# Performance work log

Hardware: AMD Instinct MI355X
Metric: run time of the kernel (lower is better)

The kernel has to match this reference:

```python
import jax, jax.numpy as jnp
import numpy as np

B, P, H, A = 256, 196, 1024, 512

def setup_inputs() -> dict:
    key = jax.random.key(0)
    ks = jax.random.split(key, 20)
    s = 1.0 / np.sqrt(H)
    sa = 1.0 / np.sqrt(A)
    return {
        "spatial_image": jax.random.normal(ks[0], (B, P, H), jnp.float32),
        "decoder_out": jax.random.normal(ks[1], (B, H), jnp.float32),
        "st": jax.random.normal(ks[2], (B, H), jnp.float32),
        "W_sen_aff": jax.random.uniform(ks[3], (H, H), jnp.float32, -s, s),
        "b_sen_aff": jax.random.uniform(ks[4], (H,), jnp.float32, -s, s),
        "W_sen_att": jax.random.uniform(ks[5], (H, A), jnp.float32, -s, s),
        "b_sen_att": jax.random.uniform(ks[6], (A,), jnp.float32, -s, s),
        "W_h_aff": jax.random.uniform(ks[7], (H, H), jnp.float32, -s, s),
        "b_h_aff": jax.random.uniform(ks[8], (H,), jnp.float32, -s, s),
        "W_h_att": jax.random.uniform(ks[9], (H, A), jnp.float32, -s, s),
        "b_h_att": jax.random.uniform(ks[10], (A,), jnp.float32, -s, s),
        "W_v_att": jax.random.uniform(ks[11], (H, A), jnp.float32, -s, s),
        "b_v_att": jax.random.uniform(ks[12], (A,), jnp.float32, -s, s),
        "W_alpha": jax.random.uniform(ks[13], (A, 1), jnp.float32, -sa, sa),
        "b_alpha": jax.random.uniform(ks[14], (1,), jnp.float32, -sa, sa),
        "W_ctx": jax.random.uniform(ks[15], (H, H), jnp.float32, -s, s),
        "b_ctx": jax.random.uniform(ks[16], (H,), jnp.float32, -s, s),
    }

def reference(spatial_image, decoder_out, st,
              W_sen_aff, b_sen_aff, W_sen_att, b_sen_att,
              W_h_aff, b_h_aff, W_h_att, b_h_att,
              W_v_att, b_v_att, W_alpha, b_alpha, W_ctx, b_ctx):
    # visual_attn: [B, P, A]
    visual_attn = jnp.einsum('bph,ha->bpa', spatial_image, W_v_att) + b_v_att
    # sentinel path: [B, H] -> relu affine -> [B, A]
    sentinel_affine = jax.nn.relu(st @ W_sen_aff + b_sen_aff)
    sentinel_attn = sentinel_affine @ W_sen_att + b_sen_att
    # hidden path: [B, H] -> tanh affine -> [B, A]
    hidden_affine = jnp.tanh(decoder_out @ W_h_aff + b_h_aff)
    hidden_attn = hidden_affine @ W_h_att + b_h_att
    # concat sentinel as an extra "pixel": [B, P+1, H] and [B, P+1, A]
    concat_features = jnp.concatenate([spatial_image, sentinel_affine[:, None, :]], axis=1)
    attended_features = jnp.concatenate([visual_attn, sentinel_attn[:, None, :]], axis=1)
    attention = jnp.tanh(attended_features + hidden_attn[:, None, :])  # [B, P+1, A]
    alpha = (jnp.einsum('bpa,ao->bpo', attention, W_alpha) + b_alpha)[..., 0]  # [B, P+1]
    att_weights = jax.nn.softmax(alpha, axis=1)
    context = jnp.einsum('bph,bp->bh', concat_features, att_weights)  # [B, H]
    beta_value = att_weights[:, -1:]  # [B, 1]
    out_l = jnp.tanh((context + hidden_affine) @ W_ctx + b_ctx)  # [B, H]
    return (out_l, att_weights, beta_value)
```

## Files before the change

kernel.cpp:

```cpp
#include <hip/hip_runtime.h>
#include <hip/hip_bf16.h>
#include <stdint.h>
#include <stddef.h>

typedef __attribute__((ext_vector_type(4))) float f32x4;
typedef __attribute__((ext_vector_type(8))) short short8;

#define MROWS 50176


static __device__ __forceinline__ int lds_off(int row, int k) {
    int slot = (k >> 3) ^ ((row >> 1) & 3);
    return (row << 6) + (slot << 4) + ((k & 7) << 1);
}

static __device__ __forceinline__ unsigned div196(unsigned g) {
    return (unsigned)(((unsigned long long)g * 85599ull) >> 24);
}

static __device__ __forceinline__ unsigned short f2bf(float f) {
    union { float f; unsigned u; } v; v.f = f;
    unsigned r = v.u + 0x7FFFu + ((v.u >> 16) & 1u);
    return (unsigned short)(r >> 16);
}

static __device__ __forceinline__ unsigned long long pack4bf(f32x4 a) {
    union { unsigned long long u; __hip_bfloat162 h[2]; } r;
    r.h[0] = __float22bfloat162_rn(make_float2(a[0], a[1]));
    r.h[1] = __float22bfloat162_rn(make_float2(a[2], a[3]));
    return r.u;
}

static __device__ __forceinline__ float tanh_fast(float x) {
    float xc = fminf(fmaxf(x, -9.f), 9.f);
    float e = __builtin_amdgcn_exp2f(xc * 2.885390081777927f);
    return (e - 1.f) * __builtin_amdgcn_rcpf(e + 1.f);
}

static __device__ __forceinline__ void gload_lds16(const void* g, void* l) {
    __builtin_amdgcn_global_load_lds(
        (const __attribute__((address_space(1))) unsigned int*)g,
        (__attribute__((address_space(3))) unsigned int*)l, 16, 0, 0);
}

__global__ __launch_bounds__(512, 2) void attn_alpha_kernel(
    const float* __restrict__ spatial,
    const unsigned short* __restrict__ WvT,
    const float* __restrict__ b_v_att,
    const float* __restrict__ hidden_attn,
    const float* __restrict__ W_alpha,
    float* __restrict__ alphab)
{
    __shared__ char sA[2][8192];
    __shared__ char sB[2][32768];
    float* alpha_s = (float*)&sA[0][0];
    const int tid = threadIdx.x;
    const int row0 = blockIdx.x << 7;

    const int lane = tid & 63, w = tid >> 6;
    const int wr = w >> 2, wc = w & 3;
    const int lrow = lane & 15, lk = lane >> 4;

    const int arow = tid >> 3;
    const int acol = (tid & 7) << 2;
    const float* Ap = spatial + (size_t)(row0 + arow) * 1024 + acol;
    const int aoff0 = lds_off(arow, acol);
    const int aoff1 = lds_off(arow + 64, acol);

    const int kg = (lane & 3) ^ ((lane >> 3) & 3);
    const unsigned short* Bp = WvT + (size_t)((w << 4) + (lane >> 2)) * 1024 + (kg << 3);

    f32x4 acc[4][8];
    f32x4 z = {0.f, 0.f, 0.f, 0.f};
    #pragma unroll
    for (int m = 0; m < 4; ++m)
        #pragma unroll
        for (int n = 0; n < 8; ++n) acc[m][n] = z;

    {
        f32x4 a0 = *(const f32x4*)(Ap);
        f32x4 a1 = *(const f32x4*)(Ap + 64 * 1024);
        #pragma unroll
        for (int r = 0; r < 4; ++r)
            gload_lds16(Bp + ((size_t)r << 17), sB[0] + (r << 13) + (w << 10));
        *(unsigned long long*)(sA[0] + aoff0) = pack4bf(a0);
        *(unsigned long long*)(sA[0] + aoff1) = pack4bf(a1);
    }
    __syncthreads();

    int cur = 0;
    #pragma unroll 1
    for (int ks = 0; ks < 32; ++ks) {
        const int nxt = cur ^ 1;
        f32x4 a0n, a1n;
        if (ks < 31) {
            const float* Apk = Ap + ((ks + 1) << 5);
            a0n = *(const f32x4*)(Apk);
            a1n = *(const f32x4*)(Apk + 64 * 1024);
            const unsigned short* Bpk = Bp + ((ks + 1) << 5);
            #pragma unroll
            for (int r = 0; r < 4; ++r)
                gload_lds16(Bpk + ((size_t)r << 17), sB[nxt] + (r << 13) + (w << 10));
        }
        short8 af[4], bf[8];
        #pragma unroll
        for (int m = 0; m < 4; ++m)
            af[m] = *(const short8*)(sA[cur] + lds_off((wr << 6) + (m << 4) + lrow, lk << 3));
        #pragma unroll
        for (int n = 0; n < 8; ++n)
            bf[n] = *(const short8*)(sB[cur] + lds_off((wc << 7) + (n << 4) + lrow, lk << 3));
        __builtin_amdgcn_s_setprio(1);
        #pragma unroll
        for (int m = 0; m < 4; ++m)
            #pragma unroll
            for (int n = 0; n < 8; ++n)
                acc[m][n] = __builtin_amdgcn_mfma_f32_16x16x32_bf16(af[m], bf[n], acc[m][n], 0, 0, 0);
        __builtin_amdgcn_s_setprio(0);
        if (ks < 31) {
            *(unsigned long long*)(sA[nxt] + aoff0) = pack4bf(a0n);
            *(unsigned long long*)(sA[nxt] + aoff1) = pack4bf(a1n);
        }
        __syncthreads();
        cur = nxt;
    }

    if (tid < 128) alpha_s[tid] = 0.f;
    __syncthreads();

    const unsigned bb0 = div196((unsigned)row0);
    const unsigned bb1 = div196((unsigned)(row0 + 127));
    float bv[8], wa[8], h0[8], h1[8];
    #pragma unroll
    for (int n = 0; n < 8; ++n) {
        int g = (wc << 7) + (n << 4) + lrow;
        bv[n] = b_v_att[g];
        wa[n] = W_alpha[g];
        h0[n] = hidden_attn[bb0 * 512 + g];
        h1[n] = hidden_attn[bb1 * 512 + g];
    }
    #pragma unroll
    for (int m = 0; m < 4; ++m) {
        int rloc0 = (wr << 6) + (m << 4) + (lk << 2);
        #pragma unroll
        for (int i = 0; i < 4; ++i) {
            unsigned g = (unsigned)(row0 + rloc0 + i);
            bool first = (div196(g) == bb0);
            float s = 0.f;
            #pragma unroll
            for (int n = 0; n < 8; ++n) {
                float v = tanh_fast(acc[m][n][i] + bv[n] + (first ? h0[n] : h1[n]));
                s += v * wa[n];
            }
            #pragma unroll
            for (int off = 1; off < 16; off <<= 1) s += __shfl_xor(s, off);
            if (lrow == 0) atomicAdd(&alpha_s[rloc0 + i], s);
        }
    }
    __syncthreads();
    if (tid < 128) {
        unsigned g = (unsigned)(row0 + tid);
        unsigned bb = div196(g);
        unsigned p = g - bb * 196;
        alphab[bb * 196 + p] = alpha_s[tid];
    }
}

static __device__ __forceinline__ void kloop_dbuf(
    const float* __restrict__ Abase,
    const unsigned short* __restrict__ Bbase,
    char* sA0, char* sA1, char* sB0, char* sB1,
    f32x4 acc[4][4], int tid)
{
    const int lane = tid & 63, w = tid >> 6;
    const int lrow = lane & 15, lk = lane >> 4;
    const int wr = w >> 1, wc = w & 1;

    const float* Ap[4];
    int aoff[4];
    #pragma unroll
    for (int r = 0; r < 4; ++r) {
        int q = tid + (r << 8);
        int ar = q >> 3, kc = (q & 7) << 2;
        Ap[r] = Abase + (size_t)ar * 1024 + kc;
        aoff[r] = lds_off(ar, kc);
    }
    const unsigned short* Bp[2];
    int bdst[2];
    #pragma unroll
    for (int c = 0; c < 2; ++c) {
        int ch = (w << 1) + c;
        int row = (ch << 4) + (lane >> 2);
        int kg = (lane & 3) ^ ((row >> 1) & 3);
        Bp[c] = Bbase + (size_t)row * 1024 + (kg << 3);
        bdst[c] = ch << 10;
    }

    f32x4 z = {0.f, 0.f, 0.f, 0.f};
    #pragma unroll
    for (int m = 0; m < 4; ++m)
        #pragma unroll
        for (int n = 0; n < 4; ++n) acc[m][n] = z;

    {
        f32x4 a[4];
        #pragma unroll
        for (int r = 0; r < 4; ++r) a[r] = *(const f32x4*)Ap[r];
        #pragma unroll
        for (int c = 0; c < 2; ++c) gload_lds16(Bp[c], sB0 + bdst[c]);
        #pragma unroll
        for (int r = 0; r < 4; ++r)
            *(unsigned long long*)(sA0 + aoff[r]) = pack4bf(a[r]);
    }
    __syncthreads();

    char* sAc = sA0; char* sAn = sA1;
    char* sBc = sB0; char* sBn = sB1;
    for (int ks = 0; ks < 32; ++ks) {
        f32x4 an[4];
        if (ks < 31) {
            const int ko = (ks + 1) << 5;
            #pragma unroll
            for (int r = 0; r < 4; ++r) an[r] = *(const f32x4*)(Ap[r] + ko);
            #pragma unroll
            for (int c = 0; c < 2; ++c) gload_lds16(Bp[c] + ko, sBn + bdst[c]);
        }
        short8 af[4], bf[4];
        #pragma unroll
        for (int m = 0; m < 4; ++m)
            af[m] = *(const short8*)(sAc + lds_off((wr << 6) + (m << 4) + lrow, lk << 3));
        #pragma unroll
        for (int n = 0; n < 4; ++n)
            bf[n] = *(const short8*)(sBc + lds_off((wc << 6) + (n << 4) + lrow, lk << 3));
        #pragma unroll
        for (int m = 0; m < 4; ++m)
            #pragma unroll
            for (int n = 0; n < 4; ++n)
                acc[m][n] = __builtin_amdgcn_mfma_f32_16x16x32_bf16(af[m], bf[n], acc[m][n], 0, 0, 0);
        if (ks < 31) {
            #pragma unroll
            for (int r = 0; r < 4; ++r)
                *(unsigned long long*)(sAn + aoff[r]) = pack4bf(an[r]);
        }
        __syncthreads();
        char* t;
        t = sAc; sAc = sAn; sAn = t;
        t = sBc; sBc = sBn; sBn = t;
    }
}

struct GemmDesc { const float* A; const unsigned short* BT; const float* bias; float* C; int N; int act; };
struct GemmPair { GemmDesc d[2]; };

__global__ __launch_bounds__(256, 4) void gemm_pair_kernel(GemmPair p)
{
    GemmDesc d = p.d[blockIdx.z];
    __shared__ char sA[2][8192];
    __shared__ char sB[2][8192];
    const int tid = threadIdx.x;
    const int row0 = blockIdx.x << 7;
    const int col0 = blockIdx.y << 7;
    f32x4 acc[4][4];
    kloop_dbuf(d.A + (size_t)row0 * 1024, d.BT + (size_t)col0 * 1024,
               sA[0], sA[1], sB[0], sB[1], acc, tid);
    const int lane = tid & 63, w = tid >> 6;
    const int wr = w >> 1, wc = w & 1;
    const int lrow = lane & 15, lk = lane >> 4;
    #pragma unroll
    for (int n = 0; n < 4; ++n) {
        int col = col0 + (wc << 6) + (n << 4) + lrow;
        float bs = d.bias[col];
        #pragma unroll
        for (int m = 0; m < 4; ++m) {
            int rbase = row0 + (wr << 6) + (m << 4) + (lk << 2);
            #pragma unroll
            for (int i = 0; i < 4; ++i) {
                float v = acc[m][n][i] + bs;
                if (d.act == 1) v = fmaxf(v, 0.f);
                if (d.act == 2) v = tanh_fast(v);
                d.C[(size_t)(rbase + i) * d.N + col] = v;
            }
        }
    }
}

struct TransDesc { const float* src; unsigned short* dst; int K; int N; };
struct TransArgs { TransDesc d[6]; };

__global__ void transpose_cvt_kernel(TransArgs args) {
    TransDesc d = args.d[blockIdx.y];
    int nt = d.N >> 5;
    int tiles = (d.K >> 5) * nt;
    if ((int)blockIdx.x >= tiles) return;
    int tk = blockIdx.x / nt, tn = blockIdx.x % nt;
    __shared__ unsigned short tile[32][33];
    int tx = threadIdx.x & 31, ty = threadIdx.x >> 5;
    int k0 = tk << 5, n0 = tn << 5;
    #pragma unroll
    for (int j = 0; j < 4; ++j)
        tile[ty + j * 8][tx] = f2bf(d.src[(size_t)(k0 + ty + j * 8) * d.N + n0 + tx]);
    __syncthreads();
    #pragma unroll
    for (int j = 0; j < 4; ++j)
        d.dst[(size_t)(n0 + ty + j * 8) * d.K + k0 + tx] = tile[tx][ty + j * 8];
}

__global__ void softmax_sentinel_kernel(
    const float* __restrict__ alphab,
    const float* __restrict__ sen_att, const float* __restrict__ hid_att,
    const float* __restrict__ W_alpha,
    float* __restrict__ att, float* __restrict__ beta)
{
    int b = blockIdx.x, tid = threadIdx.x;
    __shared__ float al[197];
    __shared__ float red[4];
    if (tid < 196) al[tid] = alphab[b * 196 + tid];
    float s = 0.f;
    for (int a = tid; a < 512; a += 256)
        s += tanh_fast(sen_att[b * 512 + a] + hid_att[b * 512 + a]) * W_alpha[a];
    #pragma unroll
    for (int off = 1; off < 64; off <<= 1) s += __shfl_xor(s, off);
    if ((tid & 63) == 0) red[tid >> 6] = s;
    __syncthreads();
    if (tid == 0) al[196] = red[0] + red[1] + red[2] + red[3];
    __syncthreads();
    if (tid < 64) {
        float v[4];
        float mx = -1e30f;
        #pragma unroll
        for (int jj = 0; jj < 4; ++jj) {
            int i = tid + jj * 64;
            v[jj] = (i < 197) ? al[i] : -1e30f;
            mx = fmaxf(mx, v[jj]);
        }
        #pragma unroll
        for (int off = 1; off < 64; off <<= 1) mx = fmaxf(mx, __shfl_xor(mx, off));
        float sm = 0.f;
        #pragma unroll
        for (int jj = 0; jj < 4; ++jj) {
            v[jj] = __builtin_amdgcn_exp2f((v[jj] - mx) * 1.442695040888963f);
            if (tid + jj * 64 >= 197) v[jj] = 0.f;
            sm += v[jj];
        }
        #pragma unroll
        for (int off = 1; off < 64; off <<= 1) sm += __shfl_xor(sm, off);
        float inv = 1.f / sm;
        #pragma unroll
        for (int jj = 0; jj < 4; ++jj) {
            int i = tid + jj * 64;
            if (i < 197) {
                float wv = v[jj] * inv;
                att[b * 197 + i] = wv;
                if (i == 196) beta[b] = wv;
            }
        }
    }
}

__global__ __launch_bounds__(256) void context_kernel(
    const float* __restrict__ spatial, const float* __restrict__ sen_aff,
    const float* __restrict__ hid_aff, const float* __restrict__ att,
    float* __restrict__ ctxh)
{
    int b = blockIdx.x, half = blockIdx.y, t = threadIdx.x;
    __shared__ float wsm[197];
    if (t < 197) wsm[t] = att[b * 197 + t];
    __syncthreads();
    int h2 = (half << 8) + t;
    const float2* sp = (const float2*)(spatial + (size_t)b * 196 * 1024) + h2;
    float ax = 0.f, ay = 0.f;
    #pragma unroll 8
    for (int p = 0; p < 196; ++p) {
        float2 x = sp[(size_t)p * 512];
        ax += wsm[p] * x.x; ay += wsm[p] * x.y;
    }
    float w196 = wsm[196];
    float2 sa = ((const float2*)(sen_aff + (size_t)b * 1024))[h2];
    float2 ha = ((const float2*)(hid_aff + (size_t)b * 1024))[h2];
    ctxh[(size_t)b * 1024 + 2 * h2]     = ax + w196 * sa.x + ha.x;
    ctxh[(size_t)b * 1024 + 2 * h2 + 1] = ay + w196 * sa.y + ha.y;
}

extern "C" void kernel_launch(void* const* d_in, const int* in_sizes, int n_in,
                              void* d_out, int out_size, void* d_ws, size_t ws_size,
                              hipStream_t stream)
{
    const float* spatial   = (const float*)d_in[0];
    const float* decoder   = (const float*)d_in[1];
    const float* st        = (const float*)d_in[2];
    const float* W_sen_aff = (const float*)d_in[3];
    const float* b_sen_aff = (const float*)d_in[4];
    const float* W_sen_att = (const float*)d_in[5];
    const float* b_sen_att = (const float*)d_in[6];
    const float* W_h_aff   = (const float*)d_in[7];
    const float* b_h_aff   = (const float*)d_in[8];
    const float* W_h_att   = (const float*)d_in[9];
    const float* b_h_att   = (const float*)d_in[10];
    const float* W_v_att   = (const float*)d_in[11];
    const float* b_v_att   = (const float*)d_in[12];
    const float* W_alpha   = (const float*)d_in[13];
    const float* W_ctx     = (const float*)d_in[15];
    const float* b_ctx     = (const float*)d_in[16];

    char* ws = (char*)d_ws;
    size_t off = 0;
    auto alloc = [&](size_t bytes) {
        char* p = ws + off; off += (bytes + 255) & ~(size_t)255; return p;
    };
    unsigned short* WvT  = (unsigned short*)alloc((size_t)512 * 1024 * 2);
    unsigned short* WsaT = (unsigned short*)alloc((size_t)1024 * 1024 * 2);
    unsigned short* WstT = (unsigned short*)alloc((size_t)512 * 1024 * 2);
    unsigned short* WhaT = (unsigned short*)alloc((size_t)1024 * 1024 * 2);
    unsigned short* WhtT = (unsigned short*)alloc((size_t)512 * 1024 * 2);
    unsigned short* WcxT = (unsigned short*)alloc((size_t)1024 * 1024 * 2);
    float* sen_aff = (float*)alloc((size_t)256 * 1024 * 4);
    float* sen_att = (float*)alloc((size_t)256 * 512 * 4);
    float* hid_aff = (float*)alloc((size_t)256 * 1024 * 4);
    float* hid_att = (float*)alloc((size_t)256 * 512 * 4);
    float* alphab  = (float*)alloc((size_t)MROWS * 4);
    float* ctxh    = (float*)alloc((size_t)256 * 1024 * 4);

    float* out_l    = (float*)d_out;
    float* out_att  = out_l + 256 * 1024;
    float* out_beta = out_att + 256 * 197;

    TransArgs ta;
    ta.d[0] = { W_v_att,   WvT,  1024, 512  };
    ta.d[1] = { W_sen_aff, WsaT, 1024, 1024 };
    ta.d[2] = { W_sen_att, WstT, 1024, 512  };
    ta.d[3] = { W_h_aff,   WhaT, 1024, 1024 };
    ta.d[4] = { W_h_att,   WhtT, 1024, 512  };
    ta.d[5] = { W_ctx,     WcxT, 1024, 1024 };
    transpose_cvt_kernel<<<dim3(1024, 6), 256, 0, stream>>>(ta);

    GemmPair p1;
    p1.d[0] = { st,      WsaT, b_sen_aff, sen_aff, 1024, 1 };
    p1.d[1] = { decoder, WhaT, b_h_aff,   hid_aff, 1024, 2 };
    gemm_pair_kernel<<<dim3(2, 8, 2), 256, 0, stream>>>(p1);

    GemmPair p2;
    p2.d[0] = { sen_aff, WstT, b_sen_att, sen_att, 512, 0 };
    p2.d[1] = { hid_aff, WhtT, b_h_att,   hid_att, 512, 0 };
    gemm_pair_kernel<<<dim3(2, 4, 2), 256, 0, stream>>>(p2);

    attn_alpha_kernel<<<392, 512, 0, stream>>>(spatial, WvT, b_v_att, hid_att, W_alpha, alphab);
    softmax_sentinel_kernel<<<256, 256, 0, stream>>>(alphab, sen_att, hid_att, W_alpha, out_att, out_beta);
    context_kernel<<<dim3(256, 2), 256, 0, stream>>>(spatial, sen_aff, hid_aff, out_att, ctxh);

    GemmPair p3;
    p3.d[0] = { ctxh, WcxT, b_ctx, out_l, 1024, 2 };
    p3.d[1] = { ctxh, WcxT, b_ctx, out_l, 1024, 2 };
    gemm_pair_kernel<<<dim3(2, 8, 1), 256, 0, stream>>>(p3);
}
```

Baseline: 240.5 us.

## Shrink attn_alpha tile to 32 rows with register-staged B and more blocks

The visual-attention GEMM block tile drops from 128 to 32 rows, so the grid grows from 392 to 1568 blocks and occupancy is raised to 4 blocks per CU. B (the weight tile) is now staged through registers into a single LDS buffer instead of double-buffered async global-to-LDS loads, and the priority hints are removed, adding an extra barrier per k-step. The aim is to fill more CUs and overlap better, but each block now re-reads the full weight slice per 32 rows, which quadruples weight traffic and lowers MFMA reuse per LDS load.

```diff
diff --git a/kernel.cpp b/kernel.cpp
--- a/kernel.cpp
+++ b/kernel.cpp
@@ -22,6 +22,12 @@
     union { float f; unsigned u; } v; v.f = f;
     unsigned r = v.u + 0x7FFFu + ((v.u >> 16) & 1u);
     return (unsigned short)(r >> 16);
+}
+
+static __device__ __forceinline__ unsigned pack2bf(float2 a) {
+    union { unsigned u; __hip_bfloat162 h; } r;
+    r.h = __float22bfloat162_rn(a);
+    return r.u;
 }
 
 static __device__ __forceinline__ unsigned long long pack4bf(f32x4 a) {
@@ -43,7 +49,7 @@
         (__attribute__((address_space(3))) unsigned int*)l, 16, 0, 0);
 }
 
-__global__ __launch_bounds__(512, 2) void attn_alpha_kernel(
+__global__ __launch_bounds__(512, 4) void attn_alpha_kernel(
     const float* __restrict__ spatial,
     const unsigned short* __restrict__ WvT,
     const float* __restrict__ b_v_att,
@@ -51,113 +57,112 @@
     const float* __restrict__ W_alpha,
     float* __restrict__ alphab)
 {
-    __shared__ char sA[2][8192];
-    __shared__ char sB[2][32768];
+    __shared__ char sA[2][2048];
+    __shared__ char sB[32768];
     float* alpha_s = (float*)&sA[0][0];
     const int tid = threadIdx.x;
-    const int row0 = blockIdx.x << 7;
+    const int row0 = blockIdx.x << 5;
 
     const int lane = tid & 63, w = tid >> 6;
-    const int wr = w >> 2, wc = w & 3;
     const int lrow = lane & 15, lk = lane >> 4;
 
-    const int arow = tid >> 3;
-    const int acol = (tid & 7) << 2;
+    const int arow = tid >> 4;
+    const int acol = (tid & 15) << 1;
     const float* Ap = spatial + (size_t)(row0 + arow) * 1024 + acol;
-    const int aoff0 = lds_off(arow, acol);
-    const int aoff1 = lds_off(arow + 64, acol);
-
-    const int kg = (lane & 3) ^ ((lane >> 3) & 3);
-    const unsigned short* Bp = WvT + (size_t)((w << 4) + (lane >> 2)) * 1024 + (kg << 3);
-
-    f32x4 acc[4][8];
+    const int aoff = lds_off(arow, acol);
+
+    const unsigned short* Bq[4];
+    int boff[4];
+    #pragma unroll
+    for (int c = 0; c < 4; ++c) {
+        int row = (c << 7) + (w << 4) + (lane >> 2);
+        int ke = (lane & 3) << 3;
+        Bq[c] = WvT + (size_t)row * 1024 + ke;
+        boff[c] = lds_off(row, ke);
+    }
+
+    f32x4 acc[2][4];
     f32x4 z = {0.f, 0.f, 0.f, 0.f};
     #pragma unroll
-    for (int m = 0; m < 4; ++m)
-        #pragma unroll
-        for (int n = 0; n < 8; ++n) acc[m][n] = z;
+    for (int m = 0; m < 2; ++m)
+        #pragma unroll
+        for (int n = 0; n < 4; ++n) acc[m][n] = z;
 
     {
-        f32x4 a0 = *(const f32x4*)(Ap);
-        f32x4 a1 = *(const f32x4*)(Ap + 64 * 1024);
-        #pragma unroll
-        for (int r = 0; r < 4; ++r)
-            gload_lds16(Bp + ((size_t)r << 17), sB[0] + (r << 13) + (w << 10));
-        *(unsigned long long*)(sA[0] + aoff0) = pack4bf(a0);
-        *(unsigned long long*)(sA[0] + aoff1) = pack4bf(a1);
-    }
-    __syncthreads();
-
-    int cur = 0;
-    #pragma unroll 1
+        float2 a0 = *(const float2*)Ap;
+        f32x4 b0[4];
+        #pragma unroll
+        for (int c = 0; c < 4; ++c) b0[c] = *(const f32x4*)Bq[c];
+        *(unsigned*)(sA[0] + aoff) = pack2bf(a0);
+        #pragma unroll
+        for (int c = 0; c < 4; ++c) *(f32x4*)(sB + boff[c]) = b0[c];
+    }
+    __syncthreads();
+
     for (int ks = 0; ks < 32; ++ks) {
-        const int nxt = cur ^ 1;
-        f32x4 a0n, a1n;
+        const int cur = ks & 1, nxt = cur ^ 1;
+        float2 aN;
+        f32x4 bN[4];
         if (ks < 31) {
-            const float* Apk = Ap + ((ks + 1) << 5);
-            a0n = *(const f32x4*)(Apk);
-            a1n = *(const f32x4*)(Apk + 64 * 1024);
-            const unsigned short* Bpk = Bp + ((ks + 1) << 5);
-            #pragma unroll
-            for (int r = 0; r < 4; ++r)
-                gload_lds16(Bpk + ((size_t)r << 17), sB[nxt] + (r << 13) + (w << 10));
-        }
-        short8 af[4], bf[8];
-        #pragma unroll
-        for (int m = 0; m < 4; ++m)
-            af[m] = *(const short8*)(sA[cur] + lds_off((wr << 6) + (m << 4) + lrow, lk << 3));
-        #pragma unroll
-        for (int n = 0; n < 8; ++n)
-            bf[n] = *(const short8*)(sB[cur] + lds_off((wc << 7) + (n << 4) + lrow, lk << 3));
-        __builtin_amdgcn_s_setprio(1);
-        #pragma unroll
-        for (int m = 0; m < 4; ++m)
-            #pragma unroll
-            for (int n = 0; n < 8; ++n)
+            const int ko = (ks + 1) << 5;
+            aN = *(const float2*)(Ap + ko);
+            #pragma unroll
+            for (int c = 0; c < 4; ++c) bN[c] = *(const f32x4*)(Bq[c] + ko);
+        }
+        short8 af[2], bf[4];
+        #pragma unroll
+        for (int m = 0; m < 2; ++m)
+            af[m] = *(const short8*)(sA[cur] + lds_off((m << 4) + lrow, lk << 3));
+        #pragma unroll
+        for (int n = 0; n < 4; ++n)
+            bf[n] = *(const short8*)(sB + lds_off((w << 6) + (n << 4) + lrow, lk << 3));
+        #pragma unroll
+        for (int m = 0; m < 2; ++m)
+            #pragma unroll
+            for (int n = 0; n < 4; ++n)
                 acc[m][n] = __builtin_amdgcn_mfma_f32_16x16x32_bf16(af[m], bf[n], acc[m][n], 0, 0, 0);
-        __builtin_amdgcn_s_setprio(0);
+        __syncthreads();
         if (ks < 31) {
-            *(unsigned long long*)(sA[nxt] + aoff0) = pack4bf(a0n);
-            *(unsigned long long*)(sA[nxt] + aoff1) = pack4bf(a1n);
-        }
-        __syncthreads();
-        cur = nxt;
-    }
-
-    if (tid < 128) alpha_s[tid] = 0.f;
+            *(unsigned*)(sA[nxt] + aoff) = pack2bf(aN);
+            #pragma unroll
+            for (int c = 0; c < 4; ++c) *(f32x4*)(sB + boff[c]) = bN[c];
+            __syncthreads();
+        }
+    }
+
+    if (tid < 32) alpha_s[tid] = 0.f;
     __syncthreads();
 
     const unsigned bb0 = div196((unsigned)row0);
-    const unsigned bb1 = div196((unsigned)(row0 + 127));
-    float bv[8], wa[8], h0[8], h1[8];
-    #pragma unroll
-    for (int n = 0; n < 8; ++n) {
-        int g = (wc << 7) + (n << 4) + lrow;
+    const unsigned bb1 = div196((unsigned)(row0 + 31));
+    float bv[4], wa[4], h0[4], h1[4];
+    #pragma unroll
+    for (int n = 0; n < 4; ++n) {
+        int g = (w << 6) + (n << 4) + lrow;
         bv[n] = b_v_att[g];
         wa[n] = W_alpha[g];
         h0[n] = hidden_attn[bb0 * 512 + g];
         h1[n] = hidden_attn[bb1 * 512 + g];
     }
     #pragma unroll
-    for (int m = 0; m < 4; ++m) {
-        int rloc0 = (wr << 6) + (m << 4) + (lk << 2);
+    for (int m = 0; m < 2; ++m) {
         #pragma unroll
         for (int i = 0; i < 4; ++i) {
-            unsigned g = (unsigned)(row0 + rloc0 + i);
-            bool first = (div196(g) == bb0);
+            int rloc = (m << 4) + (lk << 2) + i;
+            bool first = (div196((unsigned)(row0 + rloc)) == bb0);
             float s = 0.f;
             #pragma unroll
-            for (int n = 0; n < 8; ++n) {
+            for (int n = 0; n < 4; ++n) {
                 float v = tanh_fast(acc[m][n][i] + bv[n] + (first ? h0[n] : h1[n]));
                 s += v * wa[n];
             }
             #pragma unroll
             for (int off = 1; off < 16; off <<= 1) s += __shfl_xor(s, off);
-            if (lrow == 0) atomicAdd(&alpha_s[rloc0 + i], s);
-        }
-    }
-    __syncthreads();
-    if (tid < 128) {
+            if (lrow == 0) atomicAdd(&alpha_s[rloc], s);
+        }
+    }
+    __syncthreads();
+    if (tid < 32) {
         unsigned g = (unsigned)(row0 + tid);
         unsigned bb = div196(g);
         unsigned p = g - bb * 196;
@@ -442,7 +447,7 @@
     p2.d[1] = { hid_aff, WhtT, b_h_att,   hid_att, 512, 0 };
     gemm_pair_kernel<<<dim3(2, 4, 2), 256, 0, stream>>>(p2);
 
-    attn_alpha_kernel<<<392, 512, 0, stream>>>(spatial, WvT, b_v_att, hid_att, W_alpha, alphab);
+    attn_alpha_kernel<<<1568, 512, 0, stream>>>(spatial, WvT, b_v_att, hid_att, W_alpha, alphab);
     softmax_sentinel_kernel<<<256, 256, 0, stream>>>(alphab, sen_att, hid_att, W_alpha, out_att, out_beta);
     context_kernel<<<dim3(256, 2), 256, 0, stream>>>(spatial, sen_aff, hid_aff, out_att, ctxh);
 
```

Measured after the change: 259.4 us. +7.9%, slower.
